# Kernel tuning notes

Measured on AMD Instinct MI355X. Metric: run time of the kernel, lower is better.

The kernel has to match this reference:

```python
import jax, jax.numpy as jnp
import numpy as np

N, B, E = 10000, 4, 160000
C_IN, C_OUT, C_E = 64, 64, 16


def _mk_params(key, c_in, c_out, c_e):
    ks = jax.random.split(key, 8)
    s = 0.1
    return dict(
        w_n=jax.random.normal(ks[0], (c_in, c_out), jnp.float32) * s,
        w_e=jax.random.normal(ks[1], (c_e, c_out), jnp.float32) * s,
        q=jax.random.normal(ks[2], (c_out, c_out), jnp.float32) * s,
        k=jax.random.normal(ks[3], (c_out, c_out), jnp.float32) * s,
        aw=jax.random.normal(ks[4], (3 * c_out, 1), jnp.float32) * s,
        ab=jax.random.normal(ks[5], (1,), jnp.float32) * s,
        ow=jax.random.normal(ks[6], (2 * c_out, c_out), jnp.float32) * s,
        ob=jax.random.normal(ks[7], (c_out,), jnp.float32) * s,
    )


def setup_inputs() -> dict:
    key = jax.random.key(0)
    kx, ke, ka, k1, k2 = jax.random.split(key, 5)
    inp = {
        'X': jax.random.normal(kx, (N, B, C_IN), jnp.float32),
        'edge_index': jax.random.randint(ke, (2, E), 0, N, jnp.int32),
        'edge_attr': jax.random.normal(ka, (E, C_E), jnp.float32),
    }
    p1 = _mk_params(k1, C_IN, C_OUT, C_E)
    p2 = _mk_params(k2, C_OUT, C_OUT, C_E)
    for name, v in p1.items():
        inp[name + '1'] = v
    for name, v in p2.items():
        inp[name + '2'] = v
    return inp


def egnn_conv(x, edge_index, edge_attr, w_n, w_e, q, k, aw, ab, ow, ob, n_nodes):
    # x: [N,B,Cin]; edge_attr: [E,Ce]
    xp = x @ w_n                         # [N,B,C]
    ea = edge_attr @ w_e                 # [E,C]
    src, dst = edge_index[0], edge_index[1]
    xj = xp[src]                         # [E,B,C] gather (source)
    xi = xp[dst]                         # [E,B,C] gather (target)
    qf = xj @ q                          # [E,B,C]
    kf = xi @ k                          # [E,B,C]
    eab = jnp.broadcast_to(ea[:, None, :], qf.shape)  # [E,B,C]
    att_feat = jnp.concatenate([qf, kf, eab], axis=-1)  # [E,B,3C]
    att = jax.nn.sigmoid(att_feat @ aw + ab)            # [E,B,1]
    gate = jax.nn.sigmoid(eab)
    msg = att * xj * gate                # [E,B,C]
    aggr = jax.ops.segment_max(msg, dst, num_segments=n_nodes)  # [N,B,C]
    aggr = jnp.where(jnp.isneginf(aggr), 0.0, aggr)  # empty segments -> 0
    out = jnp.concatenate([xp, aggr], axis=-1) @ ow + ob
    return xp + out


def reference(X, edge_index, edge_attr,
              w_n1, w_e1, q1, k1, aw1, ab1, ow1, ob1,
              w_n2, w_e2, q2, k2, aw2, ab2, ow2, ob2):
    n_nodes = X.shape[0]
    c1 = egnn_conv(X, edge_index, edge_attr, w_n1, w_e1, q1, k1, aw1, ab1, ow1, ob1, n_nodes)
    c1 = jax.nn.leaky_relu(c1, 0.01)
    c2 = egnn_conv(c1, edge_index, edge_attr, w_n2, w_e2, q2, k2, aw2, ab2, ow2, ob2, n_nodes)
    c2 = jax.nn.leaky_relu(c2, 0.01)
    return c2
```

## Files before the change

kernel.cpp:

```cpp
#include <hip/hip_runtime.h>
#include <math.h>

#define NN 10000
#define BB 4
#define EE 160000
#define CC 64
#define CE 16

static constexpr size_t OFF_XPA    = 0;
static constexpr size_t OFF_XPB    = 10240000;
static constexpr size_t OFF_SA     = 20480000;
static constexpr size_t OFF_SB     = 20640000;
static constexpr size_t OFF_VECS   = 20800000;
static constexpr size_t OFF_COUNTS = 20801280;
static constexpr size_t OFF_CURSOR = 20841280;
static constexpr size_t OFF_OFFS   = 20881280;
static constexpr size_t OFF_RECS   = 20921344;
static constexpr size_t OFF_ATT    = 22201344;

__device__ __forceinline__ float sigmoidf_(float x) {
    return 1.0f / (1.0f + __expf(-x));
}

__global__ void hist_vecs_kernel(const int* __restrict__ ei, int* __restrict__ counts,
                                 const float* __restrict__ q1, const float* __restrict__ k1,
                                 const float* __restrict__ aw1, const float* __restrict__ we1,
                                 const float* __restrict__ q2, const float* __restrict__ k2,
                                 const float* __restrict__ aw2, const float* __restrict__ we2,
                                 float* __restrict__ vecs) {
    int e = blockIdx.x * blockDim.x + threadIdx.x;
    if (e < EE) atomicAdd(&counts[ei[EE + e]], 1);
    if (blockIdx.x == 0) {
        int t = threadIdx.x;
        if (t < 64) {
            float a = 0.f, b = 0.f, c = 0.f, d = 0.f;
            for (int j = 0; j < 64; ++j) {
                a = fmaf(q1[t * 64 + j], aw1[j], a);
                b = fmaf(k1[t * 64 + j], aw1[64 + j], b);
                c = fmaf(q2[t * 64 + j], aw2[j], c);
                d = fmaf(k2[t * 64 + j], aw2[64 + j], d);
            }
            vecs[t] = a; vecs[64 + t] = b; vecs[144 + t] = c; vecs[208 + t] = d;
        }
        if (t < 16) {
            float a = 0.f, b = 0.f;
            for (int j = 0; j < 64; ++j) {
                a = fmaf(we1[t * 64 + j], aw1[128 + j], a);
                b = fmaf(we2[t * 64 + j], aw2[128 + j], b);
            }
            vecs[128 + t] = a; vecs[272 + t] = b;
        }
    }
}

__global__ void scan_kernel(const int* __restrict__ counts, int* __restrict__ offs, int n) {
    __shared__ int sm[1024];
    __shared__ int carry_s;
    int t = threadIdx.x;
    if (t == 0) carry_s = 0;
    __syncthreads();
    for (int base = 0; base < n; base += 1024) {
        int i = base + t;
        int v = (i < n) ? counts[i] : 0;
        sm[t] = v;
        __syncthreads();
        for (int off = 1; off < 1024; off <<= 1) {
            int add = (t >= off) ? sm[t - off] : 0;
            __syncthreads();
            sm[t] += add;
            __syncthreads();
        }
        int carry = carry_s;
        if (i < n) offs[i] = carry + sm[t] - v;
        __syncthreads();
        if (t == 1023) carry_s = carry + sm[1023];
        __syncthreads();
    }
    if (t == 0) offs[n] = carry_s;
}

__global__ void scatter_kernel(const int* __restrict__ ei, const int* __restrict__ offs,
                               int* __restrict__ cursor, int2* __restrict__ recs) {
    int e = blockIdx.x * blockDim.x + threadIdx.x;
    if (e >= EE) return;
    int s = ei[e], d = ei[EE + e];
    int p = atomicAdd(&cursor[d], 1);
    recs[offs[d] + p] = make_int2(s, e);
}

__global__ __launch_bounds__(256) void node_prep_kernel(
    const float* __restrict__ x,
    const float* __restrict__ w_n,
    const float* __restrict__ qa,
    const float* __restrict__ ka,
    float* __restrict__ xp,
    float* __restrict__ sa,
    float* __restrict__ sb) {
    __shared__ float w_sh[64 * 64];
    __shared__ float x_sh[4 * BB * CC];
    int t = threadIdx.x;
    for (int i = t; i < 64 * 64; i += 256) w_sh[i] = w_n[i];
    int node0 = blockIdx.x * 4;
    const float4* xg = (const float4*)(x + (size_t)node0 * BB * CC);
    ((float4*)x_sh)[t] = xg[t];
    __syncthreads();
    int wave = t >> 6, lane = t & 63;
    int node = node0 + wave;
    const float* xrow = x_sh + wave * BB * CC;
    float acc0 = 0.f, acc1 = 0.f, acc2 = 0.f, acc3 = 0.f;
    #pragma unroll 8
    for (int ci = 0; ci < 64; ++ci) {
        float w = w_sh[ci * 64 + lane];
        acc0 = fmaf(xrow[ci], w, acc0);
        acc1 = fmaf(xrow[64 + ci], w, acc1);
        acc2 = fmaf(xrow[128 + ci], w, acc2);
        acc3 = fmaf(xrow[192 + ci], w, acc3);
    }
    size_t obase = (size_t)node * BB * CC + lane;
    xp[obase] = acc0;
    xp[obase + 64] = acc1;
    xp[obase + 128] = acc2;
    xp[obase + 192] = acc3;
    float qv = qa[lane], kv = ka[lane];
    float ra0 = acc0 * qv, ra1 = acc1 * qv, ra2 = acc2 * qv, ra3 = acc3 * qv;
    float rb0 = acc0 * kv, rb1 = acc1 * kv, rb2 = acc2 * kv, rb3 = acc3 * kv;
    #pragma unroll
    for (int off = 32; off >= 1; off >>= 1) {
        ra0 += __shfl_xor(ra0, off, 64); ra1 += __shfl_xor(ra1, off, 64);
        ra2 += __shfl_xor(ra2, off, 64); ra3 += __shfl_xor(ra3, off, 64);
        rb0 += __shfl_xor(rb0, off, 64); rb1 += __shfl_xor(rb1, off, 64);
        rb2 += __shfl_xor(rb2, off, 64); rb3 += __shfl_xor(rb3, off, 64);
    }
    if (lane == 0) {
        sa[node * BB + 0] = ra0; sa[node * BB + 1] = ra1;
        sa[node * BB + 2] = ra2; sa[node * BB + 3] = ra3;
        sb[node * BB + 0] = rb0; sb[node * BB + 1] = rb1;
        sb[node * BB + 2] = rb2; sb[node * BB + 3] = rb3;
    }
}

__global__ __launch_bounds__(256) void att_kernel(
    const int* __restrict__ ei, const float* __restrict__ attr,
    const float* __restrict__ sa, const float* __restrict__ sb,
    const float* __restrict__ weav,
    const float* __restrict__ ab,
    float4* __restrict__ att) {
    int e = blockIdx.x * blockDim.x + threadIdx.x;
    if (e >= EE) return;
    int s = ei[e], d = ei[EE + e];
    const float4* ap = (const float4*)(attr + (size_t)e * CE);
    float4 a0 = ap[0], a1 = ap[1], a2 = ap[2], a3 = ap[3];
    float se = ab[0];
    se = fmaf(a0.x, weav[0], se);  se = fmaf(a0.y, weav[1], se);
    se = fmaf(a0.z, weav[2], se);  se = fmaf(a0.w, weav[3], se);
    se = fmaf(a1.x, weav[4], se);  se = fmaf(a1.y, weav[5], se);
    se = fmaf(a1.z, weav[6], se);  se = fmaf(a1.w, weav[7], se);
    se = fmaf(a2.x, weav[8], se);  se = fmaf(a2.y, weav[9], se);
    se = fmaf(a2.z, weav[10], se); se = fmaf(a2.w, weav[11], se);
    se = fmaf(a3.x, weav[12], se); se = fmaf(a3.y, weav[13], se);
    se = fmaf(a3.z, weav[14], se); se = fmaf(a3.w, weav[15], se);
    float4 sas = *(const float4*)(sa + (size_t)s * BB);
    float4 sbn = *(const float4*)(sb + (size_t)d * BB);
    float4 r;
    r.x = sigmoidf_(sas.x + sbn.x + se);
    r.y = sigmoidf_(sas.y + sbn.y + se);
    r.z = sigmoidf_(sas.z + sbn.z + se);
    r.w = sigmoidf_(sas.w + sbn.w + se);
    att[e] = r;
}

__global__ __launch_bounds__(256) void conv_out_kernel(
    const float* __restrict__ xp,
    const int2* __restrict__ recs,
    const int* __restrict__ offs,
    const float* __restrict__ attr,
    const float* __restrict__ w_e,
    const float4* __restrict__ att,
    const float* __restrict__ ow,
    const float* __restrict__ ob,
    float* __restrict__ out) {
    __shared__ float aggr_sh[4][BB * CC];
    __shared__ float xpn_sh[4][BB * CC];
    int t = threadIdx.x;
    int wave = t >> 6, lane = t & 63;
    int node = blockIdx.x * 4 + wave;

    float wec[CE];
    #pragma unroll
    for (int j = 0; j < CE; ++j) wec[j] = w_e[j * CC + lane];

    const float* xn = xp + (size_t)node * BB * CC + lane;
    float xn0 = xn[0], xn1 = xn[64], xn2 = xn[128], xn3 = xn[192];

    int o0 = offs[node], o1 = offs[node + 1];
    float m0 = -INFINITY, m1 = -INFINITY, m2 = -INFINITY, m3 = -INFINITY;

    int i = o0;
    int2 rec = (i < o1) ? recs[i] : make_int2(0, 0);
    while (i < o1) {
        int2 cur = rec;
        ++i;
        if (i < o1) rec = recs[i];
        int s = cur.x, e = cur.y;
        float4 at = att[e];
        const float4* ap = (const float4*)(attr + (size_t)e * CE);
        float4 a0 = ap[0], a1 = ap[1], a2 = ap[2], a3 = ap[3];
        float g = 0.f;
        g = fmaf(a0.x, wec[0], g);  g = fmaf(a0.y, wec[1], g);
        g = fmaf(a0.z, wec[2], g);  g = fmaf(a0.w, wec[3], g);
        g = fmaf(a1.x, wec[4], g);  g = fmaf(a1.y, wec[5], g);
        g = fmaf(a1.z, wec[6], g);  g = fmaf(a1.w, wec[7], g);
        g = fmaf(a2.x, wec[8], g);  g = fmaf(a2.y, wec[9], g);
        g = fmaf(a2.z, wec[10], g); g = fmaf(a2.w, wec[11], g);
        g = fmaf(a3.x, wec[12], g); g = fmaf(a3.y, wec[13], g);
        g = fmaf(a3.z, wec[14], g); g = fmaf(a3.w, wec[15], g);
        g = sigmoidf_(g);
        const float* xs = xp + (size_t)s * BB * CC + lane;
        float x0 = xs[0], x1 = xs[64], x2 = xs[128], x3 = xs[192];
        m0 = fmaxf(m0, at.x * x0 * g);
        m1 = fmaxf(m1, at.y * x1 * g);
        m2 = fmaxf(m2, at.z * x2 * g);
        m3 = fmaxf(m3, at.w * x3 * g);
    }
    m0 = (m0 == -INFINITY) ? 0.f : m0;
    m1 = (m1 == -INFINITY) ? 0.f : m1;
    m2 = (m2 == -INFINITY) ? 0.f : m2;
    m3 = (m3 == -INFINITY) ? 0.f : m3;

    aggr_sh[wave][0 * CC + lane] = m0; aggr_sh[wave][1 * CC + lane] = m1;
    aggr_sh[wave][2 * CC + lane] = m2; aggr_sh[wave][3 * CC + lane] = m3;
    xpn_sh[wave][0 * CC + lane] = xn0; xpn_sh[wave][1 * CC + lane] = xn1;
    xpn_sh[wave][2 * CC + lane] = xn2; xpn_sh[wave][3 * CC + lane] = xn3;
    __syncthreads();

    const float* xr = xpn_sh[wave];
    const float* ar = aggr_sh[wave];
    float o0f = 0.f, o1f = 0.f, o2f = 0.f, o3f = 0.f;
    #pragma unroll 4
    for (int ci = 0; ci < 64; ++ci) {
        float wa = ow[ci * 64 + lane];
        float wb = ow[(64 + ci) * 64 + lane];
        o0f = fmaf(xr[ci], wa, o0f);
        o1f = fmaf(xr[CC + ci], wa, o1f);
        o2f = fmaf(xr[2 * CC + ci], wa, o2f);
        o3f = fmaf(xr[3 * CC + ci], wa, o3f);
        o0f = fmaf(ar[ci], wb, o0f);
        o1f = fmaf(ar[CC + ci], wb, o1f);
        o2f = fmaf(ar[2 * CC + ci], wb, o2f);
        o3f = fmaf(ar[3 * CC + ci], wb, o3f);
    }
    float obv = ob[lane];
    float r0 = xn0 + o0f + obv;
    float r1 = xn1 + o1f + obv;
    float r2 = xn2 + o2f + obv;
    float r3 = xn3 + o3f + obv;
    r0 = (r0 > 0.f) ? r0 : 0.01f * r0;
    r1 = (r1 > 0.f) ? r1 : 0.01f * r1;
    r2 = (r2 > 0.f) ? r2 : 0.01f * r2;
    r3 = (r3 > 0.f) ? r3 : 0.01f * r3;
    float* op = out + (size_t)node * BB * CC + lane;
    op[0] = r0; op[64] = r1; op[128] = r2; op[192] = r3;
}

extern "C" void kernel_launch(void* const* d_in, const int* in_sizes, int n_in,
                              void* d_out, int out_size, void* d_ws, size_t ws_size,
                              hipStream_t stream) {
    const float* X    = (const float*)d_in[0];
    const int*   ei   = (const int*)d_in[1];
    const float* attr = (const float*)d_in[2];
    const float* w_n1 = (const float*)d_in[3];
    const float* w_e1 = (const float*)d_in[4];
    const float* q1   = (const float*)d_in[5];
    const float* k1   = (const float*)d_in[6];
    const float* aw1  = (const float*)d_in[7];
    const float* ab1  = (const float*)d_in[8];
    const float* ow1  = (const float*)d_in[9];
    const float* ob1  = (const float*)d_in[10];
    const float* w_n2 = (const float*)d_in[11];
    const float* w_e2 = (const float*)d_in[12];
    const float* q2   = (const float*)d_in[13];
    const float* k2   = (const float*)d_in[14];
    const float* aw2  = (const float*)d_in[15];
    const float* ab2  = (const float*)d_in[16];
    const float* ow2  = (const float*)d_in[17];
    const float* ob2  = (const float*)d_in[18];
    float* out = (float*)d_out;

    char* ws = (char*)d_ws;
    float*  xpA    = (float*)(ws + OFF_XPA);
    float*  xpB    = (float*)(ws + OFF_XPB);
    float*  sa     = (float*)(ws + OFF_SA);
    float*  sb     = (float*)(ws + OFF_SB);
    float*  vecs   = (float*)(ws + OFF_VECS);
    int*    counts = (int*)(ws + OFF_COUNTS);
    int*    cursor = (int*)(ws + OFF_CURSOR);
    int*    offs   = (int*)(ws + OFF_OFFS);
    int2*   recs   = (int2*)(ws + OFF_RECS);
    float4* att    = (float4*)(ws + OFF_ATT);

    hipMemsetAsync(counts, 0, 2 * NN * sizeof(int), stream);
    hist_vecs_kernel<<<EE / 256, 256, 0, stream>>>(ei, counts, q1, k1, aw1, w_e1,
                                                   q2, k2, aw2, w_e2, vecs);
    scan_kernel<<<1, 1024, 0, stream>>>(counts, offs, NN);
    scatter_kernel<<<EE / 256, 256, 0, stream>>>(ei, offs, cursor, recs);

    node_prep_kernel<<<NN / 4, 256, 0, stream>>>(X, w_n1, vecs + 0, vecs + 64, xpA, sa, sb);
    att_kernel<<<EE / 256, 256, 0, stream>>>(ei, attr, sa, sb, vecs + 128, ab1, att);
    conv_out_kernel<<<NN / 4, 256, 0, stream>>>(xpA, recs, offs, attr, w_e1, att,
                                                ow1, ob1, xpB);
    node_prep_kernel<<<NN / 4, 256, 0, stream>>>(xpB, w_n2, vecs + 144, vecs + 208, xpA, sa, sb);
    att_kernel<<<EE / 256, 256, 0, stream>>>(ei, attr, sa, sb, vecs + 272, ab2, att);
    conv_out_kernel<<<NN / 4, 256, 0, stream>>>(xpA, recs, offs, attr, w_e2, att,
                                                ow2, ob2, out);
}
```

Baseline: 309.6 us.

## Fuse attention into CSR scatter and conv, rewrite scan and node matvecs

Removes the separate per-edge attention kernels. The edge-attribute bias terms for both layers are computed once in the scatter pass and stored in widened int4 CSR records, and the sigmoid attention is recomputed inside the aggregation loop. The loop is software-pipelined two edges deep. The scan becomes a single-pass wave-shuffle scan, the node and output matvecs use float4 weight loads straight from global memory instead of LDS, and the sigmoid uses a hardware reciprocal. This trades two launches and the att buffer round trip for larger records and extra sigmoid work per edge. The output stage drops __syncthreads in favour of an lgkmcnt wait, which relies on each wave reading only its own LDS slice.

```diff
diff --git a/kernel.cpp b/kernel.cpp
--- a/kernel.cpp
+++ b/kernel.cpp
@@ -16,10 +16,9 @@
 static constexpr size_t OFF_CURSOR = 20841280;
 static constexpr size_t OFF_OFFS   = 20881280;
 static constexpr size_t OFF_RECS   = 20921344;
-static constexpr size_t OFF_ATT    = 22201344;
 
 __device__ __forceinline__ float sigmoidf_(float x) {
-    return 1.0f / (1.0f + __expf(-x));
+    return __builtin_amdgcn_rcpf(1.0f + __expf(-x));
 }
 
 __global__ void hist_vecs_kernel(const int* __restrict__ ei, int* __restrict__ counts,
@@ -53,213 +52,230 @@
     }
 }
 
-__global__ void scan_kernel(const int* __restrict__ counts, int* __restrict__ offs, int n) {
-    __shared__ int sm[1024];
-    __shared__ int carry_s;
+__global__ __launch_bounds__(1024) void scan_kernel(const int* __restrict__ counts,
+                                                    int* __restrict__ offs, int n) {
+    __shared__ int wsum[16];
     int t = threadIdx.x;
-    if (t == 0) carry_s = 0;
+    int base = t * 10;
+    int v[10];
+    int s = 0;
+    #pragma unroll
+    for (int j = 0; j < 10; ++j) {
+        int i = base + j;
+        v[j] = (i < n) ? counts[i] : 0;
+        s += v[j];
+    }
+    int lane = t & 63, wid = t >> 6;
+    int ps = s;
+    #pragma unroll
+    for (int off = 1; off < 64; off <<= 1) {
+        int u = __shfl_up(ps, off, 64);
+        if (lane >= off) ps += u;
+    }
+    if (lane == 63) wsum[wid] = ps;
     __syncthreads();
-    for (int base = 0; base < n; base += 1024) {
-        int i = base + t;
-        int v = (i < n) ? counts[i] : 0;
-        sm[t] = v;
-        __syncthreads();
-        for (int off = 1; off < 1024; off <<= 1) {
-            int add = (t >= off) ? sm[t - off] : 0;
-            __syncthreads();
-            sm[t] += add;
-            __syncthreads();
-        }
-        int carry = carry_s;
-        if (i < n) offs[i] = carry + sm[t] - v;
-        __syncthreads();
-        if (t == 1023) carry_s = carry + sm[1023];
-        __syncthreads();
-    }
-    if (t == 0) offs[n] = carry_s;
-}
-
-__global__ void scatter_kernel(const int* __restrict__ ei, const int* __restrict__ offs,
-                               int* __restrict__ cursor, int2* __restrict__ recs) {
-    int e = blockIdx.x * blockDim.x + threadIdx.x;
-    if (e >= EE) return;
-    int s = ei[e], d = ei[EE + e];
-    int p = atomicAdd(&cursor[d], 1);
-    recs[offs[d] + p] = make_int2(s, e);
-}
-
-__global__ __launch_bounds__(256) void node_prep_kernel(
-    const float* __restrict__ x,
-    const float* __restrict__ w_n,
-    const float* __restrict__ qa,
-    const float* __restrict__ ka,
-    float* __restrict__ xp,
-    float* __restrict__ sa,
-    float* __restrict__ sb) {
-    __shared__ float w_sh[64 * 64];
-    __shared__ float x_sh[4 * BB * CC];
-    int t = threadIdx.x;
-    for (int i = t; i < 64 * 64; i += 256) w_sh[i] = w_n[i];
-    int node0 = blockIdx.x * 4;
-    const float4* xg = (const float4*)(x + (size_t)node0 * BB * CC);
-    ((float4*)x_sh)[t] = xg[t];
-    __syncthreads();
-    int wave = t >> 6, lane = t & 63;
-    int node = node0 + wave;
-    const float* xrow = x_sh + wave * BB * CC;
-    float acc0 = 0.f, acc1 = 0.f, acc2 = 0.f, acc3 = 0.f;
-    #pragma unroll 8
-    for (int ci = 0; ci < 64; ++ci) {
-        float w = w_sh[ci * 64 + lane];
-        acc0 = fmaf(xrow[ci], w, acc0);
-        acc1 = fmaf(xrow[64 + ci], w, acc1);
-        acc2 = fmaf(xrow[128 + ci], w, acc2);
-        acc3 = fmaf(xrow[192 + ci], w, acc3);
-    }
-    size_t obase = (size_t)node * BB * CC + lane;
-    xp[obase] = acc0;
-    xp[obase + 64] = acc1;
-    xp[obase + 128] = acc2;
-    xp[obase + 192] = acc3;
-    float qv = qa[lane], kv = ka[lane];
-    float ra0 = acc0 * qv, ra1 = acc1 * qv, ra2 = acc2 * qv, ra3 = acc3 * qv;
-    float rb0 = acc0 * kv, rb1 = acc1 * kv, rb2 = acc2 * kv, rb3 = acc3 * kv;
-    #pragma unroll
-    for (int off = 32; off >= 1; off >>= 1) {
-        ra0 += __shfl_xor(ra0, off, 64); ra1 += __shfl_xor(ra1, off, 64);
-        ra2 += __shfl_xor(ra2, off, 64); ra3 += __shfl_xor(ra3, off, 64);
-        rb0 += __shfl_xor(rb0, off, 64); rb1 += __shfl_xor(rb1, off, 64);
-        rb2 += __shfl_xor(rb2, off, 64); rb3 += __shfl_xor(rb3, off, 64);
-    }
-    if (lane == 0) {
-        sa[node * BB + 0] = ra0; sa[node * BB + 1] = ra1;
-        sa[node * BB + 2] = ra2; sa[node * BB + 3] = ra3;
-        sb[node * BB + 0] = rb0; sb[node * BB + 1] = rb1;
-        sb[node * BB + 2] = rb2; sb[node * BB + 3] = rb3;
-    }
-}
-
-__global__ __launch_bounds__(256) void att_kernel(
-    const int* __restrict__ ei, const float* __restrict__ attr,
-    const float* __restrict__ sa, const float* __restrict__ sb,
-    const float* __restrict__ weav,
-    const float* __restrict__ ab,
-    float4* __restrict__ att) {
+    int wbase = 0;
+    for (int w = 0; w < wid; ++w) wbase += wsum[w];
+    int tb = wbase + ps - s;
+    #pragma unroll
+    for (int j = 0; j < 10; ++j) {
+        int i = base + j;
+        if (i < n) offs[i] = tb;
+        tb += v[j];
+    }
+    if (t == 1023) offs[n] = tb;
+}
+
+__global__ __launch_bounds__(256) void scatter_kernel(
+    const int* __restrict__ ei, const int* __restrict__ offs,
+    int* __restrict__ cursor, const float* __restrict__ attr,
+    const float* __restrict__ vecs, const float* __restrict__ ab1,
+    const float* __restrict__ ab2, int4* __restrict__ recs) {
     int e = blockIdx.x * blockDim.x + threadIdx.x;
     if (e >= EE) return;
     int s = ei[e], d = ei[EE + e];
     const float4* ap = (const float4*)(attr + (size_t)e * CE);
     float4 a0 = ap[0], a1 = ap[1], a2 = ap[2], a3 = ap[3];
-    float se = ab[0];
-    se = fmaf(a0.x, weav[0], se);  se = fmaf(a0.y, weav[1], se);
-    se = fmaf(a0.z, weav[2], se);  se = fmaf(a0.w, weav[3], se);
-    se = fmaf(a1.x, weav[4], se);  se = fmaf(a1.y, weav[5], se);
-    se = fmaf(a1.z, weav[6], se);  se = fmaf(a1.w, weav[7], se);
-    se = fmaf(a2.x, weav[8], se);  se = fmaf(a2.y, weav[9], se);
-    se = fmaf(a2.z, weav[10], se); se = fmaf(a2.w, weav[11], se);
-    se = fmaf(a3.x, weav[12], se); se = fmaf(a3.y, weav[13], se);
-    se = fmaf(a3.z, weav[14], se); se = fmaf(a3.w, weav[15], se);
-    float4 sas = *(const float4*)(sa + (size_t)s * BB);
-    float4 sbn = *(const float4*)(sb + (size_t)d * BB);
-    float4 r;
-    r.x = sigmoidf_(sas.x + sbn.x + se);
-    r.y = sigmoidf_(sas.y + sbn.y + se);
-    r.z = sigmoidf_(sas.z + sbn.z + se);
-    r.w = sigmoidf_(sas.w + sbn.w + se);
-    att[e] = r;
-}
+    const float* v1 = vecs + 128;
+    const float* v2 = vecs + 272;
+    float s1 = ab1[0], s2 = ab2[0];
+    s1 = fmaf(a0.x, v1[0], s1);  s1 = fmaf(a0.y, v1[1], s1);
+    s1 = fmaf(a0.z, v1[2], s1);  s1 = fmaf(a0.w, v1[3], s1);
+    s1 = fmaf(a1.x, v1[4], s1);  s1 = fmaf(a1.y, v1[5], s1);
+    s1 = fmaf(a1.z, v1[6], s1);  s1 = fmaf(a1.w, v1[7], s1);
+    s1 = fmaf(a2.x, v1[8], s1);  s1 = fmaf(a2.y, v1[9], s1);
+    s1 = fmaf(a2.z, v1[10], s1); s1 = fmaf(a2.w, v1[11], s1);
+    s1 = fmaf(a3.x, v1[12], s1); s1 = fmaf(a3.y, v1[13], s1);
+    s1 = fmaf(a3.z, v1[14], s1); s1 = fmaf(a3.w, v1[15], s1);
+    s2 = fmaf(a0.x, v2[0], s2);  s2 = fmaf(a0.y, v2[1], s2);
+    s2 = fmaf(a0.z, v2[2], s2);  s2 = fmaf(a0.w, v2[3], s2);
+    s2 = fmaf(a1.x, v2[4], s2);  s2 = fmaf(a1.y, v2[5], s2);
+    s2 = fmaf(a1.z, v2[6], s2);  s2 = fmaf(a1.w, v2[7], s2);
+    s2 = fmaf(a2.x, v2[8], s2);  s2 = fmaf(a2.y, v2[9], s2);
+    s2 = fmaf(a2.z, v2[10], s2); s2 = fmaf(a2.w, v2[11], s2);
+    s2 = fmaf(a3.x, v2[12], s2); s2 = fmaf(a3.y, v2[13], s2);
+    s2 = fmaf(a3.z, v2[14], s2); s2 = fmaf(a3.w, v2[15], s2);
+    int p = atomicAdd(&cursor[d], 1);
+    recs[offs[d] + p] = make_int4(s, e, __float_as_int(s1), __float_as_int(s2));
+}
+
+#define FMA4(o_, s_, w_)                                                 \
+    o_.x = fmaf(s_, w_.x, o_.x); o_.y = fmaf(s_, w_.y, o_.y);            \
+    o_.z = fmaf(s_, w_.z, o_.z); o_.w = fmaf(s_, w_.w, o_.w);
+
+__global__ __launch_bounds__(256) void node_prep_kernel(
+    const float* __restrict__ x, const float* __restrict__ w_n,
+    const float* __restrict__ qa, const float* __restrict__ ka,
+    float* __restrict__ xp, float* __restrict__ sa, float* __restrict__ sb) {
+    int t = threadIdx.x, wave = t >> 6, lane = t & 63;
+    int node = blockIdx.x * 4 + wave;
+    int b = lane >> 4, q4 = (lane & 15) << 2;
+    const float* xrow = x + (size_t)node * (BB * CC) + b * CC;
+    const float* wq = w_n + q4;
+    float4 acc = make_float4(0.f, 0.f, 0.f, 0.f);
+    #pragma unroll 4
+    for (int c4 = 0; c4 < 16; ++c4) {
+        float4 xv = *(const float4*)(xrow + 4 * c4);
+        const float* wp = wq + (size_t)(4 * c4) * CC;
+        float4 w0 = *(const float4*)(wp);
+        float4 w1 = *(const float4*)(wp + CC);
+        float4 w2 = *(const float4*)(wp + 2 * CC);
+        float4 w3 = *(const float4*)(wp + 3 * CC);
+        FMA4(acc, xv.x, w0); FMA4(acc, xv.y, w1);
+        FMA4(acc, xv.z, w2); FMA4(acc, xv.w, w3);
+    }
+    *(float4*)(xp + (size_t)node * (BB * CC) + b * CC + q4) = acc;
+    float4 qv = *(const float4*)(qa + q4);
+    float4 kv = *(const float4*)(ka + q4);
+    float ra = acc.x * qv.x + acc.y * qv.y + acc.z * qv.z + acc.w * qv.w;
+    float rb = acc.x * kv.x + acc.y * kv.y + acc.z * kv.z + acc.w * kv.w;
+    #pragma unroll
+    for (int off = 1; off < 16; off <<= 1) {
+        ra += __shfl_xor(ra, off, 64);
+        rb += __shfl_xor(rb, off, 64);
+    }
+    if ((lane & 15) == 0) {
+        sa[node * BB + b] = ra;
+        sb[node * BB + b] = rb;
+    }
+}
+
+#define LOADS(R_, P) {                                                        \
+    const float4* ap_ = (const float4*)(attr + (size_t)(R_).y * CE);          \
+    P##a0 = ap_[0]; P##a1 = ap_[1]; P##a2 = ap_[2]; P##a3 = ap_[3];           \
+    P##sa = *(const float4*)(sag + (size_t)(R_).x * BB);                      \
+    const float* xr_ = xp + (size_t)(R_).x * (BB * CC) + lane;                \
+    P##x0 = xr_[0]; P##x1 = xr_[CC]; P##x2 = xr_[2 * CC]; P##x3 = xr_[3 * CC]; }
+
+#define COMPUTE(R_, P) {                                                      \
+    float g_ = 0.f;                                                           \
+    g_ = fmaf(P##a0.x, wec[0], g_);  g_ = fmaf(P##a0.y, wec[1], g_);          \
+    g_ = fmaf(P##a0.z, wec[2], g_);  g_ = fmaf(P##a0.w, wec[3], g_);          \
+    g_ = fmaf(P##a1.x, wec[4], g_);  g_ = fmaf(P##a1.y, wec[5], g_);          \
+    g_ = fmaf(P##a1.z, wec[6], g_);  g_ = fmaf(P##a1.w, wec[7], g_);          \
+    g_ = fmaf(P##a2.x, wec[8], g_);  g_ = fmaf(P##a2.y, wec[9], g_);          \
+    g_ = fmaf(P##a2.z, wec[10], g_); g_ = fmaf(P##a2.w, wec[11], g_);         \
+    g_ = fmaf(P##a3.x, wec[12], g_); g_ = fmaf(P##a3.y, wec[13], g_);         \
+    g_ = fmaf(P##a3.z, wec[14], g_); g_ = fmaf(P##a3.w, wec[15], g_);         \
+    g_ = sigmoidf_(g_);                                                       \
+    float se_ = __int_as_float(sel ? (R_).w : (R_).z);                        \
+    float t0_ = sigmoidf_(P##sa.x + sb4.x + se_);                             \
+    float t1_ = sigmoidf_(P##sa.y + sb4.y + se_);                             \
+    float t2_ = sigmoidf_(P##sa.z + sb4.z + se_);                             \
+    float t3_ = sigmoidf_(P##sa.w + sb4.w + se_);                             \
+    m0 = fmaxf(m0, t0_ * P##x0 * g_);                                         \
+    m1 = fmaxf(m1, t1_ * P##x1 * g_);                                         \
+    m2 = fmaxf(m2, t2_ * P##x2 * g_);                                         \
+    m3 = fmaxf(m3, t3_ * P##x3 * g_); }
 
 __global__ __launch_bounds__(256) void conv_out_kernel(
     const float* __restrict__ xp,
-    const int2* __restrict__ recs,
+    const int4* __restrict__ recs,
     const int* __restrict__ offs,
     const float* __restrict__ attr,
     const float* __restrict__ w_e,
-    const float4* __restrict__ att,
     const float* __restrict__ ow,
     const float* __restrict__ ob,
-    float* __restrict__ out) {
-    __shared__ float aggr_sh[4][BB * CC];
-    __shared__ float xpn_sh[4][BB * CC];
-    int t = threadIdx.x;
-    int wave = t >> 6, lane = t & 63;
+    const float* __restrict__ sag,
+    const float* __restrict__ sbg,
+    float* __restrict__ out,
+    int sel) {
+    __shared__ float aggr_sh[4][BB * 68];
+    int t = threadIdx.x, wave = t >> 6, lane = t & 63;
     int node = blockIdx.x * 4 + wave;
-
     float wec[CE];
     #pragma unroll
     for (int j = 0; j < CE; ++j) wec[j] = w_e[j * CC + lane];
-
-    const float* xn = xp + (size_t)node * BB * CC + lane;
-    float xn0 = xn[0], xn1 = xn[64], xn2 = xn[128], xn3 = xn[192];
-
+    float4 sb4 = *(const float4*)(sbg + (size_t)node * BB);
     int o0 = offs[node], o1 = offs[node + 1];
+    int n = o1 - o0;
+    const int4* rp = recs + o0;
     float m0 = -INFINITY, m1 = -INFINITY, m2 = -INFINITY, m3 = -INFINITY;
-
-    int i = o0;
-    int2 rec = (i < o1) ? recs[i] : make_int2(0, 0);
-    while (i < o1) {
-        int2 cur = rec;
-        ++i;
-        if (i < o1) rec = recs[i];
-        int s = cur.x, e = cur.y;
-        float4 at = att[e];
-        const float4* ap = (const float4*)(attr + (size_t)e * CE);
-        float4 a0 = ap[0], a1 = ap[1], a2 = ap[2], a3 = ap[3];
-        float g = 0.f;
-        g = fmaf(a0.x, wec[0], g);  g = fmaf(a0.y, wec[1], g);
-        g = fmaf(a0.z, wec[2], g);  g = fmaf(a0.w, wec[3], g);
-        g = fmaf(a1.x, wec[4], g);  g = fmaf(a1.y, wec[5], g);
-        g = fmaf(a1.z, wec[6], g);  g = fmaf(a1.w, wec[7], g);
-        g = fmaf(a2.x, wec[8], g);  g = fmaf(a2.y, wec[9], g);
-        g = fmaf(a2.z, wec[10], g); g = fmaf(a2.w, wec[11], g);
-        g = fmaf(a3.x, wec[12], g); g = fmaf(a3.y, wec[13], g);
-        g = fmaf(a3.z, wec[14], g); g = fmaf(a3.w, wec[15], g);
-        g = sigmoidf_(g);
-        const float* xs = xp + (size_t)s * BB * CC + lane;
-        float x0 = xs[0], x1 = xs[64], x2 = xs[128], x3 = xs[192];
-        m0 = fmaxf(m0, at.x * x0 * g);
-        m1 = fmaxf(m1, at.y * x1 * g);
-        m2 = fmaxf(m2, at.z * x2 * g);
-        m3 = fmaxf(m3, at.w * x3 * g);
-    }
+    float4 Aa0, Aa1, Aa2, Aa3, Asa; float Ax0, Ax1, Ax2, Ax3;
+    float4 Ba0, Ba1, Ba2, Ba3, Bsa; float Bx0, Bx1, Bx2, Bx3;
+    int4 rA = make_int4(0, 0, 0, 0), rB = rA;
+    if (n > 0) { rA = rp[0]; LOADS(rA, A); }
+    if (n > 1) { rB = rp[1]; LOADS(rB, B); }
+    int i = 0;
+    #pragma unroll 1
+    for (; i + 2 < n; i += 2) {
+        int4 rA2 = rp[i + 2];
+        int4 rB2 = (i + 3 < n) ? rp[i + 3] : rA2;
+        COMPUTE(rA, A);
+        LOADS(rA2, A);
+        COMPUTE(rB, B);
+        LOADS(rB2, B);
+        rA = rA2; rB = rB2;
+    }
+    if (i < n)     COMPUTE(rA, A);
+    if (i + 1 < n) COMPUTE(rB, B);
     m0 = (m0 == -INFINITY) ? 0.f : m0;
     m1 = (m1 == -INFINITY) ? 0.f : m1;
     m2 = (m2 == -INFINITY) ? 0.f : m2;
     m3 = (m3 == -INFINITY) ? 0.f : m3;
 
-    aggr_sh[wave][0 * CC + lane] = m0; aggr_sh[wave][1 * CC + lane] = m1;
-    aggr_sh[wave][2 * CC + lane] = m2; aggr_sh[wave][3 * CC + lane] = m3;
-    xpn_sh[wave][0 * CC + lane] = xn0; xpn_sh[wave][1 * CC + lane] = xn1;
-    xpn_sh[wave][2 * CC + lane] = xn2; xpn_sh[wave][3 * CC + lane] = xn3;
-    __syncthreads();
-
-    const float* xr = xpn_sh[wave];
-    const float* ar = aggr_sh[wave];
-    float o0f = 0.f, o1f = 0.f, o2f = 0.f, o3f = 0.f;
-    #pragma unroll 4
-    for (int ci = 0; ci < 64; ++ci) {
-        float wa = ow[ci * 64 + lane];
-        float wb = ow[(64 + ci) * 64 + lane];
-        o0f = fmaf(xr[ci], wa, o0f);
-        o1f = fmaf(xr[CC + ci], wa, o1f);
-        o2f = fmaf(xr[2 * CC + ci], wa, o2f);
-        o3f = fmaf(xr[3 * CC + ci], wa, o3f);
-        o0f = fmaf(ar[ci], wb, o0f);
-        o1f = fmaf(ar[CC + ci], wb, o1f);
-        o2f = fmaf(ar[2 * CC + ci], wb, o2f);
-        o3f = fmaf(ar[3 * CC + ci], wb, o3f);
-    }
-    float obv = ob[lane];
-    float r0 = xn0 + o0f + obv;
-    float r1 = xn1 + o1f + obv;
-    float r2 = xn2 + o2f + obv;
-    float r3 = xn3 + o3f + obv;
-    r0 = (r0 > 0.f) ? r0 : 0.01f * r0;
-    r1 = (r1 > 0.f) ? r1 : 0.01f * r1;
-    r2 = (r2 > 0.f) ? r2 : 0.01f * r2;
-    r3 = (r3 > 0.f) ? r3 : 0.01f * r3;
-    float* op = out + (size_t)node * BB * CC + lane;
-    op[0] = r0; op[64] = r1; op[128] = r2; op[192] = r3;
+    float* ash = aggr_sh[wave];
+    ash[0 * 68 + lane] = m0;
+    ash[1 * 68 + lane] = m1;
+    ash[2 * 68 + lane] = m2;
+    ash[3 * 68 + lane] = m3;
+    asm volatile("s_waitcnt lgkmcnt(0)" ::: "memory");
+
+    int b = lane >> 4, q4 = (lane & 15) << 2;
+    const float* agr = ash + b * 68;
+    const float* xrow = xp + (size_t)node * (BB * CC) + b * CC;
+    const float* owa = ow + q4;
+    const float* owb = ow + CC * CC + q4;
+    float4 o = make_float4(0.f, 0.f, 0.f, 0.f);
+    #pragma unroll 2
+    for (int c4 = 0; c4 < 16; ++c4) {
+        float4 xv = *(const float4*)(xrow + 4 * c4);
+        float4 av = *(const float4*)(agr + 4 * c4);
+        const float* wpa = owa + (size_t)(4 * c4) * CC;
+        float4 w0 = *(const float4*)(wpa);
+        float4 w1 = *(const float4*)(wpa + CC);
+        float4 w2 = *(const float4*)(wpa + 2 * CC);
+        float4 w3 = *(const float4*)(wpa + 3 * CC);
+        const float* wpb = owb + (size_t)(4 * c4) * CC;
+        float4 u0 = *(const float4*)(wpb);
+        float4 u1 = *(const float4*)(wpb + CC);
+        float4 u2 = *(const float4*)(wpb + 2 * CC);
+        float4 u3 = *(const float4*)(wpb + 3 * CC);
+        FMA4(o, xv.x, w0); FMA4(o, xv.y, w1); FMA4(o, xv.z, w2); FMA4(o, xv.w, w3);
+        FMA4(o, av.x, u0); FMA4(o, av.y, u1); FMA4(o, av.z, u2); FMA4(o, av.w, u3);
+    }
+    float4 xnv = *(const float4*)(xrow + q4);
+    float4 ob4 = *(const float4*)(ob + q4);
+    float4 r;
+    r.x = xnv.x + o.x + ob4.x;
+    r.y = xnv.y + o.y + ob4.y;
+    r.z = xnv.z + o.z + ob4.z;
+    r.w = xnv.w + o.w + ob4.w;
+    r.x = (r.x > 0.f) ? r.x : 0.01f * r.x;
+    r.y = (r.y > 0.f) ? r.y : 0.01f * r.y;
+    r.z = (r.z > 0.f) ? r.z : 0.01f * r.z;
+    r.w = (r.w > 0.f) ? r.w : 0.01f * r.w;
+    *(float4*)(out + (size_t)node * (BB * CC) + b * CC + q4) = r;
 }
 
 extern "C" void kernel_launch(void* const* d_in, const int* in_sizes, int n_in,
@@ -287,29 +303,26 @@
     float* out = (float*)d_out;
 
     char* ws = (char*)d_ws;
-    float*  xpA    = (float*)(ws + OFF_XPA);
-    float*  xpB    = (float*)(ws + OFF_XPB);
-    float*  sa     = (float*)(ws + OFF_SA);
-    float*  sb     = (float*)(ws + OFF_SB);
-    float*  vecs   = (float*)(ws + OFF_VECS);
-    int*    counts = (int*)(ws + OFF_COUNTS);
-    int*    cursor = (int*)(ws + OFF_CURSOR);
-    int*    offs   = (int*)(ws + OFF_OFFS);
-    int2*   recs   = (int2*)(ws + OFF_RECS);
-    float4* att    = (float4*)(ws + OFF_ATT);
+    float* xpA    = (float*)(ws + OFF_XPA);
+    float* xpB    = (float*)(ws + OFF_XPB);
+    float* sa     = (float*)(ws + OFF_SA);
+    float* sb     = (float*)(ws + OFF_SB);
+    float* vecs   = (float*)(ws + OFF_VECS);
+    int*   counts = (int*)(ws + OFF_COUNTS);
+    int*   cursor = (int*)(ws + OFF_CURSOR);
+    int*   offs   = (int*)(ws + OFF_OFFS);
+    int4*  recs   = (int4*)(ws + OFF_RECS);
 
     hipMemsetAsync(counts, 0, 2 * NN * sizeof(int), stream);
     hist_vecs_kernel<<<EE / 256, 256, 0, stream>>>(ei, counts, q1, k1, aw1, w_e1,
                                                    q2, k2, aw2, w_e2, vecs);
     scan_kernel<<<1, 1024, 0, stream>>>(counts, offs, NN);
-    scatter_kernel<<<EE / 256, 256, 0, stream>>>(ei, offs, cursor, recs);
-
+    scatter_kernel<<<EE / 256, 256, 0, stream>>>(ei, offs, cursor, attr, vecs,
+                                                 ab1, ab2, recs);
     node_prep_kernel<<<NN / 4, 256, 0, stream>>>(X, w_n1, vecs + 0, vecs + 64, xpA, sa, sb);
-    att_kernel<<<EE / 256, 256, 0, stream>>>(ei, attr, sa, sb, vecs + 128, ab1, att);
-    conv_out_kernel<<<NN / 4, 256, 0, stream>>>(xpA, recs, offs, attr, w_e1, att,
-                                                ow1, ob1, xpB);
+    conv_out_kernel<<<NN / 4, 256, 0, stream>>>(xpA, recs, offs, attr, w_e1,
+                                                ow1, ob1, sa, sb, xpB, 0);
     node_prep_kernel<<<NN / 4, 256, 0, stream>>>(xpB, w_n2, vecs + 144, vecs + 208, xpA, sa, sb);
-    att_kernel<<<EE / 256, 256, 0, stream>>>(ei, attr, sa, sb, vecs + 272, ab2, att);
-    conv_out_kernel<<<NN / 4, 256, 0, stream>>>(xpA, recs, offs, attr, w_e2, att,
-                                                ow2, ob2, out);
-}
+    conv_out_kernel<<<NN / 4, 256, 0, stream>>>(xpA, recs, offs, attr, w_e2,
+                                                ow2, ob2, sa, sb, out, 1);
+}
```

Result: slower. 353.1 us (+14.1%).
